# Kernel optimization log

Hardware: AMD Instinct MI355X
Metric: run time of the kernel (lower is better)

The kernel has to match this reference:

```python
import jax, jax.numpy as jnp
import numpy as np

N_CARD, N_TX, N_MER = 100_000, 1_000_000, 10_000
E = 1_000_000
H = 128


def setup_inputs() -> dict:
    key = jax.random.key(0)
    ks = iter(jax.random.split(key, 32))
    nrm = lambda shape, s=1.0: jax.random.normal(next(ks), shape, jnp.float32) * s
    W = 0.05  # weight scale for numerical sanity across two relu layers
    inp = {
        "x_card": nrm((N_CARD, 32)),
        "x_tx": nrm((N_TX, 64)),
        "x_mer": nrm((N_MER, 32)),
        # layer-1 SAGEConv params per edge type: lin_l (src->H, w/ bias), lin_r (dst->H)
        "l1_pays_wl": nrm((32, H), W), "l1_pays_bl": nrm((H,), W), "l1_pays_wr": nrm((64, H), W),
        "l1_recv_wl": nrm((32, H), W), "l1_recv_bl": nrm((H,), W), "l1_recv_wr": nrm((64, H), W),
        "l1_rpays_wl": nrm((64, H), W), "l1_rpays_bl": nrm((H,), W), "l1_rpays_wr": nrm((32, H), W),
        "l1_rrecv_wl": nrm((64, H), W), "l1_rrecv_bl": nrm((H,), W), "l1_rrecv_wr": nrm((32, H), W),
        # layer-2: all relations are H->H; stacked in order [pays, receives, rev_pays, rev_receives]
        "w2l": nrm((4, H, H), W), "b2": nrm((4, H), W), "w2r": nrm((4, H, H), W),
        # final lazy Linear(-1, out_channels=1) -> (H, 1)
        "wf": nrm((H, 1), W), "bf": nrm((1,), W),
        "pays_src": jax.random.randint(next(ks), (E,), 0, N_CARD, jnp.int32),
        "pays_dst": jnp.arange(E, dtype=jnp.int32),
        "recv_src": jax.random.randint(next(ks), (E,), 0, N_MER, jnp.int32),
        "recv_dst": jnp.arange(E, dtype=jnp.int32),
    }
    return inp


def _sage(x_src, x_dst, src, dst, wl, bl, wr, n_dst):
    """PyG SAGEConv(aggr='mean'): lin_l(mean_j x_j) + lin_r(x_root)."""
    msg = x_src[src]  # [E, d_src] gather
    s = jax.ops.segment_sum(msg, dst, num_segments=n_dst)
    cnt = jax.ops.segment_sum(jnp.ones((src.shape[0], 1), msg.dtype), dst, num_segments=n_dst)
    mean = s / jnp.maximum(cnt, 1.0)
    return mean @ wl + bl + x_dst @ wr


def reference(x_card, x_tx, x_mer,
              l1_pays_wl, l1_pays_bl, l1_pays_wr,
              l1_recv_wl, l1_recv_bl, l1_recv_wr,
              l1_rpays_wl, l1_rpays_bl, l1_rpays_wr,
              l1_rrecv_wl, l1_rrecv_bl, l1_rrecv_wr,
              w2l, b2, w2r, wf, bf,
              pays_src, pays_dst, recv_src, recv_dst):
    # ---- layer 1 (HeteroConv aggr='sum' over relations sharing a dst type) ----
    tx = (_sage(x_card, x_tx, pays_src, pays_dst, l1_pays_wl, l1_pays_bl, l1_pays_wr, N_TX)
          + _sage(x_mer, x_tx, recv_src, recv_dst, l1_recv_wl, l1_recv_bl, l1_recv_wr, N_TX))
    # rev_pays / rev_receives are the transposed edge lists
    card = _sage(x_tx, x_card, pays_dst, pays_src, l1_rpays_wl, l1_rpays_bl, l1_rpays_wr, N_CARD)
    mer = _sage(x_tx, x_mer, recv_dst, recv_src, l1_rrecv_wl, l1_rrecv_bl, l1_rrecv_wr, N_MER)
    tx, card, mer = jax.nn.relu(tx), jax.nn.relu(card), jax.nn.relu(mer)
    # ---- layer 2 (only transaction output feeds the head; card/mer layer-2 outputs unused) ----
    tx2 = (_sage(card, tx, pays_src, pays_dst, w2l[0], b2[0], w2r[0], N_TX)
           + _sage(mer, tx, recv_src, recv_dst, w2l[1], b2[1], w2r[1], N_TX))
    tx2 = jax.nn.relu(tx2)
    return tx2 @ wf + bf  # [N_TX, 1]
```

## Files before the change

kernel.cpp:

```cpp
#include <hip/hip_runtime.h>
#include <hip/hip_bf16.h>
#include <stdint.h>

#define NCARD 100000
#define NTX   1000000
#define NMER  10000
#define NE    1000000
#define CAPC  48
#define CAPM  192
#define NCB   3125
#define NMB   313


typedef __attribute__((ext_vector_type(8))) short bf16x8;
typedef __attribute__((ext_vector_type(4))) float f32x4;

__device__ inline unsigned short f2bf(float f) {
  union { float f; uint32_t u; } v; v.f = f;
  uint32_t r = v.u + 0x7FFF + ((v.u >> 16) & 1);
  return (unsigned short)(r >> 16);
}
__device__ inline float bf2f(unsigned short u) {
  union { uint32_t u; float f; } v; v.u = ((uint32_t)u) << 16;
  return v.f;
}
__device__ inline uint32_t addpack2(uint32_t a, uint32_t b) {
  float lo = bf2f((unsigned short)(a & 0xffff)) + bf2f((unsigned short)(b & 0xffff));
  float hi = bf2f((unsigned short)(a >> 16))   + bf2f((unsigned short)(b >> 16));
  return (uint32_t)f2bf(lo) | ((uint32_t)f2bf(hi) << 16);
}

#define OFF_WR1T  0u
#define OFF_W2RT  4096u
#define OFF_B1    12288u
#define OFF_B2    12416u
#define OFF_CW1   12544u
#define OFF_CW2   18688u
#define OFF_CW3   26880u
#define OFF_MW1   28928u
#define OFF_MW2   35072u
#define OFF_MW3   43264u
#define OFF_CQ    45312u
#define OFF_MQ    12845312u
#define OFF_CCNT  14125312u
#define OFF_MCNT  14225312u
#define OFF_CBUK  14235312u
#define OFF_MBUK  19035312u
#define OFF_XB    20955312u
#define WS_END    52955312u

__global__ __launch_bounds__(256) void k_prep_all(
    const float* __restrict__ pays_wr, const float* __restrict__ recv_wr,
    const float* __restrict__ w2r, const float* __restrict__ pays_bl,
    const float* __restrict__ recv_bl, const float* __restrict__ b2,
    unsigned short* __restrict__ wr1t, unsigned short* __restrict__ w2rt,
    float* __restrict__ b1sum, float* __restrict__ b2sum,
    const float* __restrict__ c_wl64, const float* __restrict__ c_wr32,
    const float* __restrict__ c_w2, const float* __restrict__ c_wg,
    unsigned short* __restrict__ cw1, unsigned short* __restrict__ cw2,
    unsigned short* __restrict__ cw3,
    const float* __restrict__ m_wl64, const float* __restrict__ m_wr32,
    const float* __restrict__ m_w2, const float* __restrict__ m_wg,
    unsigned short* __restrict__ mw1, unsigned short* __restrict__ mw2,
    unsigned short* __restrict__ mw3)
{
  const int grp = blockIdx.x >> 6;
  const int i = (blockIdx.x & 63) * 256 + threadIdx.x;
  if (grp == 0) {
    if (i < 8192) {
      int n = i >> 6, k = i & 63;
      wr1t[i] = f2bf(pays_wr[k * 128 + n] + recv_wr[k * 128 + n]);
    }
    if (i < 16384) {
      int n = i >> 7, k = i & 127;
      w2rt[i] = f2bf(w2r[k * 128 + n] + w2r[16384 + k * 128 + n]);
    }
    if (i < 128) {
      b1sum[i] = pays_bl[i] + recv_bl[i];
      b2sum[i] = b2[i] + b2[128 + i];
    }
  } else {
    const float* wl64 = (grp == 1) ? c_wl64 : m_wl64;
    const float* wr32 = (grp == 1) ? c_wr32 : m_wr32;
    const float* w2   = (grp == 1) ? c_w2   : m_w2;
    const float* wg   = (grp == 1) ? c_wg   : m_wg;
    unsigned short* w1t = (grp == 1) ? cw1 : mw1;
    unsigned short* w2t = (grp == 1) ? cw2 : mw2;
    unsigned short* w3t = (grp == 1) ? cw3 : mw3;
    if (i < 12288) {
      int n = i / 96, k = i % 96;
      float v = (k < 64) ? wl64[k * 128 + n] : wr32[(k - 64) * 128 + n];
      w1t[i] = f2bf(v);
    }
    if (i < 16384) { int n = i >> 7, k = i & 127; w2t[i] = f2bf(w2[k * 128 + n]); }
    if (i < 4096)  { int n = i >> 5, k = i & 31;  w3t[i] = f2bf(wg[k * 128 + n]); }
  }
}

__global__ __launch_bounds__(256) void k_convert_build(
    const float* __restrict__ x, unsigned short* __restrict__ xb,
    const int* __restrict__ ps, const int* __restrict__ rs,
    int* __restrict__ ccnt, int* __restrict__ mcnt,
    int* __restrict__ cbuk, int* __restrict__ mbuk)
{
  int64_t i = (int64_t)blockIdx.x * 256 + threadIdx.x;
  if (i < 16000000) {
    float4 v = ((const float4*)x)[i];
    unsigned short p[4] = { f2bf(v.x), f2bf(v.y), f2bf(v.z), f2bf(v.w) };
    *(uint2*)&xb[i * 4] = *(const uint2*)p;
  }
  if (i < NE) {
    int e = (int)i;
    int c = ps[e];
    int pos = atomicAdd(ccnt + c, 1);
    if (pos < CAPC) cbuk[c * CAPC + pos] = e;
    int m = rs[e];
    int pm = atomicAdd(mcnt + m, 1);
    if (pm < CAPM) mbuk[m * CAPM + pm] = e;
  }
}

__global__ __launch_bounds__(256) void k_node_both(
    const int* __restrict__ ccnt, const int* __restrict__ cbuk,
    const int* __restrict__ mcnt, const int* __restrict__ mbuk,
    const unsigned short* __restrict__ xb,
    const float* __restrict__ x_card, const float* __restrict__ x_mer,
    const unsigned short* __restrict__ cw1, const unsigned short* __restrict__ cw2,
    const unsigned short* __restrict__ cw3, const float* __restrict__ cbl,
    const unsigned short* __restrict__ mw1, const unsigned short* __restrict__ mw2,
    const unsigned short* __restrict__ mw3, const float* __restrict__ mbl,
    const float* __restrict__ b1sum, const float* __restrict__ b2sum,
    unsigned short* __restrict__ cq, unsigned short* __restrict__ mq)
{
  const bool iscard = blockIdx.x < NCB;
  const int* cnt = iscard ? ccnt : mcnt;
  const int* buk = iscard ? cbuk : mbuk;
  const int cap  = iscard ? CAPC : CAPM;
  const int R    = iscard ? NCARD : NMER;
  const float* x_node = iscard ? x_card : x_mer;
  const unsigned short* w1t = iscard ? cw1 : mw1;
  const unsigned short* w2t = iscard ? cw2 : mw2;
  const unsigned short* w3t = iscard ? cw3 : mw3;
  const float* bl = iscard ? cbl : mbl;
  unsigned short* q = iscard ? cq : mq;
  const int n0 = (iscard ? blockIdx.x : blockIdx.x - NCB) * 32;

  __shared__ unsigned short ms[32 * 64];
  __shared__ unsigned short xs2[32 * 32];
  __shared__ unsigned short ts[32 * 128];
  __shared__ float bll[128], ba1[128], ba2[128];
  const int tid = threadIdx.x;
  const int wv = tid >> 6, l = tid & 63;
  const int lr = l & 15, lk = l >> 4;

  bf16x8 f1[2][3], f2w[2][4], f3[2];
#pragma unroll
  for (int c = 0; c < 2; ++c) {
    const int n = wv * 32 + c * 16 + lr;
#pragma unroll
    for (int k = 0; k < 3; ++k)
      f1[c][k] = *(const bf16x8*)(w1t + n * 96 + k * 32 + lk * 8);
#pragma unroll
    for (int k = 0; k < 4; ++k)
      f2w[c][k] = *(const bf16x8*)(w2t + n * 128 + k * 32 + lk * 8);
    f3[c] = *(const bf16x8*)(w3t + n * 32 + lk * 8);
  }
  if (tid < 128) {
    bll[tid] = bl[tid];
    ba1[tid] = iscard ? b1sum[tid] : 0.f;
    ba2[tid] = iscard ? b2sum[tid] : 0.f;
  }

  const int half = l >> 5, c32 = l & 31;
  for (int rr = wv; rr < 32; rr += 4) {
    const int node = n0 + rr;
    int deg = 0;
    if (node < R) deg = cnt[node];
    const int64_t base = (int64_t)node * cap;
    float a0 = 0.f, a1 = 0.f;
    int p = half;
    for (; p + 6 < deg; p += 8) {
      int e0 = buk[base + p],     e1 = buk[base + p + 2];
      int e2 = buk[base + p + 4], e3 = buk[base + p + 6];
      uint32_t v0 = *(const uint32_t*)&xb[(int64_t)e0 * 64 + c32 * 2];
      uint32_t v1 = *(const uint32_t*)&xb[(int64_t)e1 * 64 + c32 * 2];
      uint32_t v2 = *(const uint32_t*)&xb[(int64_t)e2 * 64 + c32 * 2];
      uint32_t v3 = *(const uint32_t*)&xb[(int64_t)e3 * 64 + c32 * 2];
      a0 += bf2f((unsigned short)(v0 & 0xffff)) + bf2f((unsigned short)(v1 & 0xffff))
          + bf2f((unsigned short)(v2 & 0xffff)) + bf2f((unsigned short)(v3 & 0xffff));
      a1 += bf2f((unsigned short)(v0 >> 16)) + bf2f((unsigned short)(v1 >> 16))
          + bf2f((unsigned short)(v2 >> 16)) + bf2f((unsigned short)(v3 >> 16));
    }
    for (; p < deg; p += 2) {
      int e = buk[base + p];
      uint32_t v = *(const uint32_t*)&xb[(int64_t)e * 64 + c32 * 2];
      a0 += bf2f((unsigned short)(v & 0xffff));
      a1 += bf2f((unsigned short)(v >> 16));
    }
    a0 += __shfl_xor(a0, 32, 64);
    a1 += __shfl_xor(a1, 32, 64);
    if (half == 0) {
      float inv = 1.f / fmaxf((float)deg, 1.f);
      unsigned short pr[2] = { f2bf(a0 * inv), f2bf(a1 * inv) };
      int li = (rr * 64 + c32 * 2) ^ ((rr & 7) << 3);
      *(uint32_t*)&ms[li] = *(const uint32_t*)pr;
    }
  }
#pragma unroll
  for (int q4 = 0; q4 < 4; ++q4) {
    int id = q4 * 256 + tid;
    int r = id >> 5, c = id & 31;
    float v = (n0 + r < R) ? x_node[(int64_t)(n0 + r) * 32 + c] : 0.f;
    xs2[(r * 32 + c) ^ ((r & 3) << 3)] = f2bf(v);
  }
  __syncthreads();

#pragma unroll
  for (int rt = 0; rt < 2; ++rt) {
    const int arow = rt * 16 + lr;
    const int sw = (arow & 7) << 3, sw2 = (arow & 3) << 3;
    bf16x8 a0 = *(const bf16x8*)&ms[(arow * 64 + 0  + lk * 8) ^ sw];
    bf16x8 a1 = *(const bf16x8*)&ms[(arow * 64 + 32 + lk * 8) ^ sw];
    bf16x8 ax = *(const bf16x8*)&xs2[(arow * 32 + lk * 8) ^ sw2];
    f32x4 acc0 = {0.f,0.f,0.f,0.f}, acc1 = {0.f,0.f,0.f,0.f};
    acc0 = __builtin_amdgcn_mfma_f32_16x16x32_bf16(a0, f1[0][0], acc0, 0, 0, 0);
    acc0 = __builtin_amdgcn_mfma_f32_16x16x32_bf16(a1, f1[0][1], acc0, 0, 0, 0);
    acc0 = __builtin_amdgcn_mfma_f32_16x16x32_bf16(ax, f1[0][2], acc0, 0, 0, 0);
    acc1 = __builtin_amdgcn_mfma_f32_16x16x32_bf16(a0, f1[1][0], acc1, 0, 0, 0);
    acc1 = __builtin_amdgcn_mfma_f32_16x16x32_bf16(a1, f1[1][1], acc1, 0, 0, 0);
    acc1 = __builtin_amdgcn_mfma_f32_16x16x32_bf16(ax, f1[1][2], acc1, 0, 0, 0);
#pragma unroll
    for (int c = 0; c < 2; ++c) {
      const int col = wv * 32 + c * 16 + lr;
#pragma unroll
      for (int i = 0; i < 4; ++i) {
        const int r = rt * 16 + lk * 4 + i;
        float v = (c ? acc1[i] : acc0[i]) + bll[col];
        ts[(r * 128 + col) ^ ((r & 7) << 3)] = f2bf(fmaxf(v, 0.f));
      }
    }
  }
  __syncthreads();

#pragma unroll
  for (int rt = 0; rt < 2; ++rt) {
    const int arow = rt * 16 + lr;
    const int sw = (arow & 7) << 3, sw2 = (arow & 3) << 3;
    f32x4 b0 = {0.f,0.f,0.f,0.f}, b1a = {0.f,0.f,0.f,0.f};
#pragma unroll
    for (int kk = 0; kk < 4; ++kk) {
      bf16x8 a = *(const bf16x8*)&ts[(arow * 128 + kk * 32 + lk * 8) ^ sw];
      b0  = __builtin_amdgcn_mfma_f32_16x16x32_bf16(a, f2w[0][kk], b0, 0, 0, 0);
      b1a = __builtin_amdgcn_mfma_f32_16x16x32_bf16(a, f2w[1][kk], b1a, 0, 0, 0);
    }
    bf16x8 ax = *(const bf16x8*)&xs2[(arow * 32 + lk * 8) ^ sw2];
    f32x4 g0 = {0.f,0.f,0.f,0.f}, g1a = {0.f,0.f,0.f,0.f};
    g0  = __builtin_amdgcn_mfma_f32_16x16x32_bf16(ax, f3[0], g0, 0, 0, 0);
    g1a = __builtin_amdgcn_mfma_f32_16x16x32_bf16(ax, f3[1], g1a, 0, 0, 0);
#pragma unroll
    for (int c = 0; c < 2; ++c) {
#pragma unroll
      for (int i = 0; i < 4; ++i) {
        const int node = n0 + rt * 16 + lk * 4 + i;
        const int col = wv * 32 + c * 16 + lr;
        if (node < R) {
          q[node * 256 + col]       = f2bf((c ? g1a[i] : g0[i]) + ba1[col]);
          q[node * 256 + 128 + col] = f2bf((c ? b1a[i] : b0[i]) + ba2[col]);
        }
      }
    }
  }
}

#define TXR 32
__global__ __launch_bounds__(256) void k_fused_tx_mfma(
    const unsigned short* __restrict__ xb,
    const int* __restrict__ ps, const int* __restrict__ rs,
    const unsigned short* __restrict__ cq, const unsigned short* __restrict__ mq,
    const unsigned short* __restrict__ wr1t, const unsigned short* __restrict__ w2rt,
    const float* __restrict__ wf, const float* __restrict__ bfp,
    float* __restrict__ out)
{
  __shared__ unsigned short xs[TXR * 64];
  __shared__ unsigned short ts[TXR * 128];
  __shared__ unsigned short g1[TXR * 128];
  __shared__ unsigned short g2[TXR * 128];
  __shared__ float partial[4][TXR];
  __shared__ float wfl[128];

  const int tid = threadIdx.x;
  const int wv = tid >> 6;
  const int l  = tid & 63;
  const int lr = l & 15;
  const int lk = l >> 4;

  bf16x8 w1f[2][2], w2f[2][4];
#pragma unroll
  for (int c = 0; c < 2; ++c) {
    const int n = (wv * 2 + c) * 16 + lr;
#pragma unroll
    for (int kk = 0; kk < 2; ++kk)
      w1f[c][kk] = *(const bf16x8*)(wr1t + n * 64 + kk * 32 + lk * 8);
#pragma unroll
    for (int kk = 0; kk < 4; ++kk)
      w2f[c][kk] = *(const bf16x8*)(w2rt + n * 128 + kk * 32 + lk * 8);
  }
  if (tid < 128) wfl[tid] = wf[tid];
  const float bfv = bfp[0];

  const uint32_t* cqd = (const uint32_t*)cq;
  const uint32_t* mqd = (const uint32_t*)mq;

  for (int64_t row0 = (int64_t)blockIdx.x * TXR; row0 < NTX;
       row0 += (int64_t)gridDim.x * TXR) {
    __syncthreads();
    {
      const int r = tid >> 3, seg = tid & 7;
      uint4 v = *(const uint4*)&xb[(row0 + r) * 64 + seg * 8];
      *(uint4*)&xs[(r * 64 + seg * 8) ^ ((r & 7) << 3)] = v;
    }
#pragma unroll
    for (int p = 0; p < 8; ++p) {
      const int r = p * 4 + wv;
      const int64_t c = ps[row0 + r];
      const int64_t m = rs[row0 + r];
      const int dst = r * 64 + (l ^ (p << 3));
      uint32_t a1 = cqd[c * 128 + l],      v1 = mqd[m * 128 + l];
      ((uint32_t*)g1)[dst] = addpack2(a1, v1);
      uint32_t a2 = cqd[c * 128 + 64 + l], v2 = mqd[m * 128 + 64 + l];
      ((uint32_t*)g2)[dst] = addpack2(a2, v2);
    }
    __syncthreads();

#pragma unroll
    for (int rt = 0; rt < 2; ++rt) {
      const int arow = rt * 16 + lr;
      const int sw = (arow & 7) << 3;
      bf16x8 a0  = *(const bf16x8*)&xs[(arow * 64 + 0  + lk * 8) ^ sw];
      bf16x8 a1v = *(const bf16x8*)&xs[(arow * 64 + 32 + lk * 8) ^ sw];
      f32x4 acc0 = {0.f,0.f,0.f,0.f}, acc1 = {0.f,0.f,0.f,0.f};
      acc0 = __builtin_amdgcn_mfma_f32_16x16x32_bf16(a0,  w1f[0][0], acc0, 0, 0, 0);
      acc0 = __builtin_amdgcn_mfma_f32_16x16x32_bf16(a1v, w1f[0][1], acc0, 0, 0, 0);
      acc1 = __builtin_amdgcn_mfma_f32_16x16x32_bf16(a0,  w1f[1][0], acc1, 0, 0, 0);
      acc1 = __builtin_amdgcn_mfma_f32_16x16x32_bf16(a1v, w1f[1][1], acc1, 0, 0, 0);
      const int gx = (rt * 4 + lk) << 3;
#pragma unroll
      for (int c = 0; c < 2; ++c) {
        const int col = wv * 32 + c * 16 + lr;
        const int gofs = (((col >> 1) ^ gx) << 1) + (col & 1);
        const f32x4 acc = c ? acc1 : acc0;
#pragma unroll
        for (int i = 0; i < 4; ++i) {
          const int r = rt * 16 + lk * 4 + i;
          float v = acc[i] + bf2f(g1[r * 128 + gofs]);
          ts[(r * 128 + col) ^ ((r & 7) << 3)] = f2bf(fmaxf(v, 0.f));
        }
      }
    }
    __syncthreads();

#pragma unroll
    for (int rt = 0; rt < 2; ++rt) {
      const int arow = rt * 16 + lr;
      const int sw = (arow & 7) << 3;
      f32x4 acc0 = {0.f,0.f,0.f,0.f}, acc1 = {0.f,0.f,0.f,0.f};
#pragma unroll
      for (int kk = 0; kk < 4; ++kk) {
        bf16x8 a = *(const bf16x8*)&ts[(arow * 128 + kk * 32 + lk * 8) ^ sw];
        acc0 = __builtin_amdgcn_mfma_f32_16x16x32_bf16(a, w2f[0][kk], acc0, 0, 0, 0);
        acc1 = __builtin_amdgcn_mfma_f32_16x16x32_bf16(a, w2f[1][kk], acc1, 0, 0, 0);
      }
      const int gx = (rt * 4 + lk) << 3;
#pragma unroll
      for (int i = 0; i < 4; ++i) {
        const int r = rt * 16 + lk * 4 + i;
        float sum = 0.f;
#pragma unroll
        for (int c = 0; c < 2; ++c) {
          const int col = wv * 32 + c * 16 + lr;
          const int gofs = (((col >> 1) ^ gx) << 1) + (col & 1);
          float y = (c ? acc1[i] : acc0[i]) + bf2f(g2[r * 128 + gofs]);
          sum = fmaf(fmaxf(y, 0.f), wfl[col], sum);
        }
#pragma unroll
        for (int off = 1; off < 16; off <<= 1) sum += __shfl_xor(sum, off, 64);
        if (lr == 0) partial[wv][r] = sum;
      }
    }
    __syncthreads();
    if (tid < TXR)
      out[row0 + tid] = partial[0][tid] + partial[1][tid] + partial[2][tid]
                      + partial[3][tid] + bfv;
  }
}

extern "C" void kernel_launch(void* const* d_in, const int* in_sizes, int n_in,
                              void* d_out, int out_size, void* d_ws, size_t ws_size,
                              hipStream_t stream) {
  const float* x_card = (const float*)d_in[0];
  const float* x_tx   = (const float*)d_in[1];
  const float* x_mer  = (const float*)d_in[2];
  const float* l1_pays_wl = (const float*)d_in[3];
  const float* l1_pays_bl = (const float*)d_in[4];
  const float* l1_pays_wr = (const float*)d_in[5];
  const float* l1_recv_wl = (const float*)d_in[6];
  const float* l1_recv_bl = (const float*)d_in[7];
  const float* l1_recv_wr = (const float*)d_in[8];
  const float* l1_rpays_wl = (const float*)d_in[9];
  const float* l1_rpays_bl = (const float*)d_in[10];
  const float* l1_rpays_wr = (const float*)d_in[11];
  const float* l1_rrecv_wl = (const float*)d_in[12];
  const float* l1_rrecv_bl = (const float*)d_in[13];
  const float* l1_rrecv_wr = (const float*)d_in[14];
  const float* w2l = (const float*)d_in[15];
  const float* b2  = (const float*)d_in[16];
  const float* w2r = (const float*)d_in[17];
  const float* wf  = (const float*)d_in[18];
  const float* bf  = (const float*)d_in[19];
  const int* pays_src = (const int*)d_in[20];
  const int* recv_src = (const int*)d_in[22];

  float* ws = (float*)d_ws;
  unsigned short* wr1t = (unsigned short*)(ws + OFF_WR1T);
  unsigned short* w2rt = (unsigned short*)(ws + OFF_W2RT);
  float* b1sum = ws + OFF_B1;
  float* b2sum = ws + OFF_B2;
  unsigned short* cw1 = (unsigned short*)(ws + OFF_CW1);
  unsigned short* cw2 = (unsigned short*)(ws + OFF_CW2);
  unsigned short* cw3 = (unsigned short*)(ws + OFF_CW3);
  unsigned short* mw1 = (unsigned short*)(ws + OFF_MW1);
  unsigned short* mw2 = (unsigned short*)(ws + OFF_MW2);
  unsigned short* mw3 = (unsigned short*)(ws + OFF_MW3);
  unsigned short* cq  = (unsigned short*)(ws + OFF_CQ);
  unsigned short* mq  = (unsigned short*)(ws + OFF_MQ);
  int* ccnt = (int*)(ws + OFF_CCNT);
  int* mcnt = (int*)(ws + OFF_MCNT);
  int* cbuk = (int*)(ws + OFF_CBUK);
  int* mbuk = (int*)(ws + OFF_MBUK);
  unsigned short* xb = (unsigned short*)(ws + OFF_XB);

  hipMemsetAsync((char*)d_ws + (size_t)OFF_CCNT * 4, 0,
                 (size_t)(OFF_CBUK - OFF_CCNT) * 4, stream);

  k_prep_all<<<192, 256, 0, stream>>>(
      l1_pays_wr, l1_recv_wr, w2r, l1_pays_bl, l1_recv_bl, b2,
      wr1t, w2rt, b1sum, b2sum,
      l1_rpays_wl, l1_rpays_wr, w2l, l1_pays_wl, cw1, cw2, cw3,
      l1_rrecv_wl, l1_rrecv_wr, w2l + 16384, l1_recv_wl, mw1, mw2, mw3);

  k_convert_build<<<62500, 256, 0, stream>>>(x_tx, xb, pays_src, recv_src,
                                             ccnt, mcnt, cbuk, mbuk);

  k_node_both<<<NCB + NMB, 256, 0, stream>>>(
      ccnt, cbuk, mcnt, mbuk, xb, x_card, x_mer,
      cw1, cw2, cw3, l1_rpays_bl,
      mw1, mw2, mw3, l1_rrecv_bl,
      b1sum, b2sum, cq, mq);

  k_fused_tx_mfma<<<2048, 256, 0, stream>>>(xb, pays_src, recv_src, cq, mq,
                                            wr1t, w2rt, wf, bf, (float*)d_out);
}
```

Baseline: 683.0 us.

## Widen conversion stores, deepen gather unroll, reorder merchant blocks, set occupancy hint

The conversion kernel now handles 8 floats per thread with 16-byte stores, halving the grid to 31250 blocks while still covering the edge bucket build (8M threads cover all 1M edges). The node kernel schedules the high-degree merchant blocks first and adds a 16-wide unrolled gather loop so more loads are in flight per wave. The fused tx kernel gets a min-blocks-per-SM launch bound of 5, which may limit registers and cause spills.

```diff
diff --git a/kernel.cpp b/kernel.cpp
--- a/kernel.cpp
+++ b/kernel.cpp
@@ -104,10 +104,12 @@
     int* __restrict__ cbuk, int* __restrict__ mbuk)
 {
   int64_t i = (int64_t)blockIdx.x * 256 + threadIdx.x;
-  if (i < 16000000) {
-    float4 v = ((const float4*)x)[i];
-    unsigned short p[4] = { f2bf(v.x), f2bf(v.y), f2bf(v.z), f2bf(v.w) };
-    *(uint2*)&xb[i * 4] = *(const uint2*)p;
+  {
+    float4 va = ((const float4*)x)[i * 2];
+    float4 vb = ((const float4*)x)[i * 2 + 1];
+    unsigned short p8[8] = { f2bf(va.x), f2bf(va.y), f2bf(va.z), f2bf(va.w),
+                             f2bf(vb.x), f2bf(vb.y), f2bf(vb.z), f2bf(vb.w) };
+    *(uint4*)&xb[i * 8] = *(const uint4*)p8;
   }
   if (i < NE) {
     int e = (int)i;
@@ -132,7 +134,7 @@
     const float* __restrict__ b1sum, const float* __restrict__ b2sum,
     unsigned short* __restrict__ cq, unsigned short* __restrict__ mq)
 {
-  const bool iscard = blockIdx.x < NCB;
+  const bool iscard = blockIdx.x >= NMB;
   const int* cnt = iscard ? ccnt : mcnt;
   const int* buk = iscard ? cbuk : mbuk;
   const int cap  = iscard ? CAPC : CAPM;
@@ -143,7 +145,7 @@
   const unsigned short* w3t = iscard ? cw3 : mw3;
   const float* bl = iscard ? cbl : mbl;
   unsigned short* q = iscard ? cq : mq;
-  const int n0 = (iscard ? blockIdx.x : blockIdx.x - NCB) * 32;
+  const int n0 = (iscard ? (blockIdx.x - NMB) : blockIdx.x) * 32;
 
   __shared__ unsigned short ms[32 * 64];
   __shared__ unsigned short xs2[32 * 32];
@@ -179,6 +181,20 @@
     const int64_t base = (int64_t)node * cap;
     float a0 = 0.f, a1 = 0.f;
     int p = half;
+    for (; p + 14 < deg; p += 16) {
+      int ei[8];
+      uint32_t vi[8];
+#pragma unroll
+      for (int u = 0; u < 8; ++u) ei[u] = buk[base + p + 2 * u];
+#pragma unroll
+      for (int u = 0; u < 8; ++u)
+        vi[u] = *(const uint32_t*)&xb[(int64_t)ei[u] * 64 + c32 * 2];
+#pragma unroll
+      for (int u = 0; u < 8; ++u) {
+        a0 += bf2f((unsigned short)(vi[u] & 0xffff));
+        a1 += bf2f((unsigned short)(vi[u] >> 16));
+      }
+    }
     for (; p + 6 < deg; p += 8) {
       int e0 = buk[base + p],     e1 = buk[base + p + 2];
       int e2 = buk[base + p + 4], e3 = buk[base + p + 6];
@@ -273,7 +289,7 @@
 }
 
 #define TXR 32
-__global__ __launch_bounds__(256) void k_fused_tx_mfma(
+__global__ __launch_bounds__(256, 5) void k_fused_tx_mfma(
     const unsigned short* __restrict__ xb,
     const int* __restrict__ ps, const int* __restrict__ rs,
     const unsigned short* __restrict__ cq, const unsigned short* __restrict__ mq,
@@ -439,8 +455,8 @@
   int* mbuk = (int*)(ws + OFF_MBUK);
   unsigned short* xb = (unsigned short*)(ws + OFF_XB);
 
-  hipMemsetAsync((char*)d_ws + (size_t)OFF_CCNT * 4, 0,
-                 (size_t)(OFF_CBUK - OFF_CCNT) * 4, stream);
+  (void)hipMemsetAsync((char*)d_ws + (size_t)OFF_CCNT * 4, 0,
+                       (size_t)(OFF_CBUK - OFF_CCNT) * 4, stream);
 
   k_prep_all<<<192, 256, 0, stream>>>(
       l1_pays_wr, l1_recv_wr, w2r, l1_pays_bl, l1_recv_bl, b2,
@@ -448,7 +464,7 @@
       l1_rpays_wl, l1_rpays_wr, w2l, l1_pays_wl, cw1, cw2, cw3,
       l1_rrecv_wl, l1_rrecv_wr, w2l + 16384, l1_recv_wl, mw1, mw2, mw3);
 
-  k_convert_build<<<62500, 256, 0, stream>>>(x_tx, xb, pays_src, recv_src,
+  k_convert_build<<<31250, 256, 0, stream>>>(x_tx, xb, pays_src, recv_src,
                                              ccnt, mcnt, cbuk, mbuk);
 
   k_node_both<<<NCB + NMB, 256, 0, stream>>>(
```

Result: slower. 1.137 ms (+66.5%).
